# Kernel tuning notes

Measured on AMD Instinct MI355X. Metric: run time of the kernel, lower is better.

## Reference

```python
import jax, jax.numpy as jnp
import numpy as np
from jax import lax

B, T, V, E, H, M = 512, 60, 50000, 300, 512, 256


def _lstm_final_h(x_emb, seqlen, kernel, bias):
    """BasicLSTMCell (gate order i,j,f,o; forget_bias=1.0) with dynamic_rnn
    sequence_length semantics: state stops updating at t >= seqlen.
    x_emb: [B, T, E]; returns final h: [B, H]."""
    b = x_emb.shape[0]
    h0 = jnp.zeros((b, H), x_emb.dtype)
    c0 = jnp.zeros((b, H), x_emb.dtype)

    def step(carry, inp):
        c, h = carry
        xt, t = inp
        z = jnp.concatenate([xt, h], axis=1) @ kernel + bias  # [B, 4H]
        i, j, f, o = jnp.split(z, 4, axis=1)
        nc = c * jax.nn.sigmoid(f + 1.0) + jax.nn.sigmoid(i) * jnp.tanh(j)
        nh = jnp.tanh(nc) * jax.nn.sigmoid(o)
        valid = (t < seqlen)[:, None]
        return (jnp.where(valid, nc, c), jnp.where(valid, nh, h)), None

    (c, h), _ = lax.scan(step, (c0, h0),
                         (jnp.swapaxes(x_emb, 0, 1), jnp.arange(T)))
    return h


def setup_inputs() -> dict:
    key = jax.random.key(0)
    ks = jax.random.split(key, 8)
    return {
        "input1": jax.random.randint(ks[0], (B, T), 0, V, dtype=jnp.int32),
        "input2": jax.random.randint(ks[1], (B, T), 0, V, dtype=jnp.int32),
        "seqlen1": jax.random.randint(ks[2], (B,), 1, T + 1, dtype=jnp.int32),
        "seqlen2": jax.random.randint(ks[3], (B,), 1, T + 1, dtype=jnp.int32),
        "embeddings": jax.random.normal(ks[4], (V, E), jnp.float32) * 0.1,
        "lstm_kernel": jax.random.normal(ks[5], (E + H, 4 * H), jnp.float32) * 0.02,
        "lstm_bias": jnp.zeros((4 * H,), jnp.float32),
        "W1": jax.random.normal(ks[6], (4 * (H + 1) + 1, M), jnp.float32) * 0.02,
        "b1": jnp.zeros((1, M), jnp.float32),
        "W2": jax.random.normal(ks[7], (M, 2), jnp.float32) * 0.02,
        "b2": jnp.zeros((1, 2), jnp.float32),
    }


def reference(input1, input2, seqlen1, seqlen2, embeddings,
              lstm_kernel, lstm_bias, W1, b1, W2, b2):
    x1 = embeddings[input1]  # [B, T, E]
    x2 = embeddings[input2]
    h1 = _lstm_final_h(x1, seqlen1, lstm_kernel, lstm_bias)  # [B, H]
    h2 = _lstm_final_h(x2, seqlen2, lstm_kernel, lstm_bias)
    len1 = (seqlen1.astype(jnp.float32) / float(T))[:, None]
    len2 = (seqlen2.astype(jnp.float32) / float(T))[:, None]
    h1 = jnp.concatenate([h1, len1], axis=1)  # [B, H+1]
    h2 = jnp.concatenate([h2, len2], axis=1)
    h_sub = h1 - h2
    h_dist = jnp.sum(h_sub * h_sub, axis=1, keepdims=True)  # [B, 1]
    h_mul = h1 * h2
    h_combined = jnp.concatenate([h1, h2, h_sub, h_dist, h_mul], axis=1)
    e1 = jax.nn.relu(h_combined @ W1 + b1)  # dropout keep_prob=1 -> identity
    preds = e1 @ W2 + b2  # [B, 2]
    return preds
```

## Files before the change

kernel.cpp:

```cpp
#include <hip/hip_runtime.h>
#include <hip/hip_bf16.h>

#define BATCH 512
#define TT 60
#define EDIM 300
#define HDIM 512
#define KP1 2112
#define MDIM 256
#define V48 2400000

typedef __bf16 bf16x4 __attribute__((ext_vector_type(4)));
typedef __bf16 bf16x8 __attribute__((ext_vector_type(8)));
typedef float  f32x16 __attribute__((ext_vector_type(16)));

#define GLL16(g, l) __builtin_amdgcn_global_load_lds( \
    (const __attribute__((address_space(1))) void*)(g), \
    (__attribute__((address_space(3))) void*)(l), 16, 0, 0)

#define SBAR()  __builtin_amdgcn_s_barrier()
#define SCHED0() __builtin_amdgcn_sched_barrier(0)

__device__ __forceinline__ float sigm(float x) {
    return 1.0f / (1.0f + __expf(-x));
}
__device__ __forceinline__ float tanh_fast(float x) {
    float e = __expf(-2.0f * fabsf(x));
    float r = (1.0f - e) / (1.0f + e);
    return x >= 0.0f ? r : -r;
}


__global__ __launch_bounds__(256) void sort_rows(const int* __restrict__ sl1,
                                                 const int* __restrict__ sl2,
                                                 int* __restrict__ rowinfo,
                                                 unsigned* __restrict__ step_done) {
    __shared__ unsigned cnt[61];
    __shared__ unsigned off[61];
    int tid = threadIdx.x;
    if (tid < 61) cnt[tid] = 0;
    if (tid >= 64 && tid < 80) step_done[tid - 64] = 0;
    __syncthreads();
    for (int i = tid; i < 1024; i += 256) {
        int sl = (i < 512) ? sl1[i] : sl2[i - 512];
        atomicAdd(&cnt[60 - sl], 1u);
    }
    __syncthreads();
    if (tid == 0) {
        unsigned s = 0;
        for (int k = 0; k < 61; ++k) { off[k] = s; s += cnt[k]; }
    }
    __syncthreads();
    for (int i = tid; i < 1024; i += 256) {
        int sc = i >= 512;
        int b = i & 511;
        int sl = sc ? sl2[b] : sl1[b];
        unsigned pos = atomicAdd(&off[60 - sl], 1u);
        rowinfo[pos] = b | (sc << 15) | (sl << 20);
    }
}

__global__ __launch_bounds__(256) void prep_w(const float* __restrict__ kern,
                                              __bf16* __restrict__ wf) {
    __shared__ float tile[64][65];
    int bk = blockIdx.x % 14;
    int bn = blockIdx.x / 14;
    int k0 = bk * 64, n0 = bn * 64;
    int tid = threadIdx.x;
#pragma unroll
    for (int i = 0; i < 16; ++i) {
        int id = i * 256 + tid;
        int kk = id >> 6, nn = id & 63;
        int kg = k0 + kk;
        int src = (kg < 300) ? kg : (kg >= 384 ? kg - 84 : -1);
        tile[kk][nn] = (src >= 0) ? kern[(size_t)src * 2048 + n0 + nn] : 0.0f;
    }
    __syncthreads();
    int gate = n0 >> 9;
    int nt = gate >> 1;
#pragma unroll
    for (int i = 0; i < 2; ++i) {
        int id = i * 256 + tid;
        int nn = id >> 3, k8 = id & 7;
        bf16x8 hv, lv;
#pragma unroll
        for (int j = 0; j < 8; ++j) {
            float v = tile[k8 * 8 + j][nn];
            __bf16 h = (__bf16)v;
            hv[j] = h;
            lv[j] = (__bf16)(v - (float)h);
        }
        int cg = (((n0 & 511) >> 4) + (nn >> 4));
        int hc = nn & 15;
        int lzc = ((gate & 1) << 4) + hc;
        int kglob = k0 + k8 * 8;
        int c = kglob >> 7;
        int j = (kglob >> 4) & 7;
        int half = k8 & 1;
        size_t o = (size_t)cg * 114688 + c * 16384 + (j * 4 + nt * 2) * 512
                 + (half * 32 + lzc) * 8;
        *(bf16x8*)(wf + o) = hv;
        *(bf16x8*)(wf + o + 512) = lv;
    }
}

__global__ __launch_bounds__(256) void prep_w1(const float* __restrict__ W1,
                                               __bf16* __restrict__ w1h,
                                               __bf16* __restrict__ w1l) {
    __shared__ float tile[64][65];
    int bk = blockIdx.x % 33;
    int bn = blockIdx.x / 33;
    int k0 = bk * 64, n0 = bn * 64;
    int tid = threadIdx.x;
#pragma unroll
    for (int i = 0; i < 16; ++i) {
        int id = i * 256 + tid;
        int kk = id >> 6, nn = id & 63;
        int kg = k0 + kk;
        tile[kk][nn] = (kg < 2053) ? W1[(size_t)kg * MDIM + n0 + nn] : 0.0f;
    }
    __syncthreads();
#pragma unroll
    for (int i = 0; i < 2; ++i) {
        int id = i * 256 + tid;
        int nn = id >> 3, k8 = (id & 7) * 8;
        bf16x8 hv, lv;
#pragma unroll
        for (int j = 0; j < 8; ++j) {
            float v = tile[k8 + j][nn];
            __bf16 h = (__bf16)v;
            hv[j] = h;
            lv[j] = (__bf16)(v - (float)h);
        }
        size_t o = (size_t)(n0 + nn) * KP1 + k0 + k8;
        *(bf16x8*)(w1h + o) = hv;
        *(bf16x8*)(w1l + o) = lv;
    }
}

__global__ __launch_bounds__(256) void prep_emb(const float* __restrict__ emb,
                                                __bf16* __restrict__ embB) {
    int id = blockIdx.x * 256 + threadIdx.x;
    if (id >= V48) return;
    int tok = id / 48;
    int k8 = id - tok * 48;
    int k0 = k8 * 8;
    float vv[8];
    const float* er = emb + (size_t)tok * EDIM + k0;
    if (k0 + 8 <= EDIM) {
        float4 f0 = *(const float4*)er;
        float4 f1 = *(const float4*)(er + 4);
        vv[0] = f0.x; vv[1] = f0.y; vv[2] = f0.z; vv[3] = f0.w;
        vv[4] = f1.x; vv[5] = f1.y; vv[6] = f1.z; vv[7] = f1.w;
    } else if (k0 < EDIM) {
        float4 f0 = *(const float4*)er;
        vv[0] = f0.x; vv[1] = f0.y; vv[2] = f0.z; vv[3] = f0.w;
        vv[4] = vv[5] = vv[6] = vv[7] = 0.f;
    } else {
#pragma unroll
        for (int j = 0; j < 8; ++j) vv[j] = 0.f;
    }
    bf16x8 hv, lv;
#pragma unroll
    for (int j = 0; j < 8; ++j) {
        __bf16 h = (__bf16)vv[j];
        hv[j] = h;
        lv[j] = (__bf16)(vv[j] - (float)h);
    }
    size_t o = (size_t)tok * 768 + k0;
    *(bf16x8*)(embB + o) = hv;
    *(bf16x8*)(embB + o + 384) = lv;
}

#define ZSTR 72

__global__ __launch_bounds__(256, 2) void lstm_all(
    const int* __restrict__ in1, const int* __restrict__ in2,
    const int* __restrict__ rowinfo,
    const __bf16* __restrict__ embB, const float* __restrict__ bias,
    const __bf16* __restrict__ wf,
    __bf16* __restrict__ XfH,
    unsigned* __restrict__ step_done,
    float* __restrict__ h_state) {

    int bx = blockIdx.x;
    int xcd = bx & 7;
    int loc = bx >> 3;
    int u = loc >> 3;
    int p = xcd & 1;
    int bt = (u < 4) ? ((u << 1) | p) : (15 - (((u - 4) << 1) | p));
    int cg = ((xcd >> 1) << 3) | (loc & 7);

    __shared__ __align__(16) __bf16 Bb[2][16384];
    __shared__ __align__(16) __bf16 zh[2048];
    __shared__ int info_s[64];

    int tid = threadIdx.x;
    int w = tid >> 6, lane = tid & 63, l31 = lane & 31;
    int s = w >> 1, kg = w & 1;

    if (tid < 64) info_s[tid] = rowinfo[bt * 64 + tid];
    __syncthreads();
    int t_end = info_s[0] >> 20;

    int rowl = s * 32 + l31;
    int inf_r = info_s[rowl];
    const int* tokptr = ((((inf_r >> 15) & 1) ? in2 : in1)) + (inf_r & 511) * TT;

    int hc16 = tid & 15;
    int hcol = (cg << 4) + hc16;
    float bi = bias[hcol], bj = bias[512 + hcol];
    float bfv = bias[1024 + hcol], bo = bias[1536 + hcol];

    float c_reg[4] = {0.f, 0.f, 0.f, 0.f};
    float h_reg[4] = {0.f, 0.f, 0.f, 0.f};

    const __bf16* wb = wf + (size_t)cg * 114688;
    auto stageB = [&](int c, int buf) {
        const __bf16* src = wb + c * 16384 + w * 4096 + lane * 8;
        __bf16* dst = &Bb[buf][w * 4096 + lane * 8];
#pragma unroll
        for (int i = 0; i < 8; ++i)
            GLL16(src + i * 512, dst + i * 512);
    };

    int ew = kg * 64 + ((lane >> 5) << 3);
    size_t hw_off = (size_t)((s * 2 + kg) * 4) * 4096 + lane * 8;

    int tok = tokptr[0];
    stageB(0, 0);
    SCHED0();
    bf16x8 aH[4], aL[4];
    const __bf16* eb = embB + (size_t)tok * 768 + ew;
#pragma unroll
    for (int jj = 0; jj < 4; ++jj) {
        aH[jj] = *(const bf16x8*)(eb + jj * 16);
        aL[jj] = *(const bf16x8*)(eb + 384 + jj * 16);
    }
    SCHED0();

    for (int t = 0; t < t_end; ++t) {
        f32x16 acc[2];
#pragma unroll
        for (int nt = 0; nt < 2; ++nt)
#pragma unroll
            for (int r = 0; r < 16; ++r) acc[nt][r] = 0.0f;

        const __bf16* hrd = XfH + ((size_t)t * 16 + bt) * 65536 + hw_off;

#pragma unroll
        for (int c = 0; c < 7; ++c) {
            int cur = (t + c) & 1;
            asm volatile("s_waitcnt vmcnt(8)" ::: "memory");
            SBAR();
            SCHED0();
            if (c == 2 && t > 0) {
                if (tid == 0) {
                    unsigned target = 32u * (unsigned)t;
                    int guard = 0;
                    while (__hip_atomic_load(step_done + bt, __ATOMIC_RELAXED,
                                             __HIP_MEMORY_SCOPE_AGENT) < target) {
                        __builtin_amdgcn_s_sleep(1);
                        if (++guard > (1 << 20)) break;
                    }
                }
                SBAR();
                SCHED0();
            }
            bf16x8 nH[4], nL[4];
            if (c < 6) {
                stageB(c + 1, 1 - cur);
                SCHED0();
                if (c < 2) {
                    const __bf16* en = eb + (c + 1) * 128;
#pragma unroll
                    for (int jj = 0; jj < 4; ++jj) {
                        nH[jj] = *(const bf16x8*)(en + jj * 16);
                        nL[jj] = *(const bf16x8*)(en + 384 + jj * 16);
                    }
                } else {
                    const __bf16* An = hrd + (c - 2) * 4096;
#pragma unroll
                    for (int jj = 0; jj < 4; ++jj) {
                        nH[jj] = *(const bf16x8*)(An + jj * 1024);
                        nL[jj] = *(const bf16x8*)(An + jj * 1024 + 512);
                    }
                }
                SCHED0();
            }
#pragma unroll
            for (int jj = 0; jj < 4; ++jj) {
                int j = kg * 4 + jj;
#pragma unroll
                for (int nt = 0; nt < 2; ++nt) {
                    int T0 = (j * 4 + nt * 2) * 512 + lane * 8;
                    bf16x8 bh = *(const bf16x8*)(&Bb[cur][T0]);
                    bf16x8 bl = *(const bf16x8*)(&Bb[cur][T0 + 512]);
                    acc[nt] = __builtin_amdgcn_mfma_f32_32x32x16_bf16(aH[jj], bh, acc[nt], 0, 0, 0);
                    acc[nt] = __builtin_amdgcn_mfma_f32_32x32x16_bf16(aH[jj], bl, acc[nt], 0, 0, 0);
                    acc[nt] = __builtin_amdgcn_mfma_f32_32x32x16_bf16(aL[jj], bh, acc[nt], 0, 0, 0);
                }
            }
            if (c < 6) {
#pragma unroll
                for (int jj = 0; jj < 4; ++jj) { aH[jj] = nH[jj]; aL[jj] = nL[jj]; }
            }
        }

        SBAR();
        SCHED0();

        int tn = (t + 1 < TT) ? t + 1 : TT - 1;
        int tok_n = tokptr[tn];
        SCHED0();

        float* zsb = (float*)&Bb[0][0];
#pragma unroll
        for (int nt = 0; nt < 2; ++nt)
#pragma unroll
            for (int r = 0; r < 16; ++r) {
                int rl = s * 32 + (r & 3) + ((r >> 2) << 3) + ((lane >> 5) << 2);
                zsb[kg * 4608 + rl * ZSTR + nt * 32 + l31] = acc[nt][r];
            }
        asm volatile("s_waitcnt lgkmcnt(0)" ::: "memory");
        SBAR();
        SCHED0();

#pragma unroll
        for (int i = 0; i < 4; ++i) {
            int rl = i * 16 + (tid >> 4);
            int info = info_s[rl];
            int sl = info >> 20;
            float zi = zsb[rl * ZSTR + hc16]      + zsb[4608 + rl * ZSTR + hc16]      + bi;
            float zj = zsb[rl * ZSTR + 16 + hc16] + zsb[4608 + rl * ZSTR + 16 + hc16] + bj;
            float zf = zsb[rl * ZSTR + 32 + hc16] + zsb[4608 + rl * ZSTR + 32 + hc16] + bfv;
            float zo = zsb[rl * ZSTR + 48 + hc16] + zsb[4608 + rl * ZSTR + 48 + hc16] + bo;
            float c_old = c_reg[i];
            float h_old = h_reg[i];
            float nc = c_old * sigm(zf + 1.0f) + sigm(zi) * tanh_fast(zj);
            float nh = tanh_fast(nc) * sigm(zo);
            bool valid = t < sl;
            float cs = valid ? nc : c_old;
            float hs = valid ? nh : h_old;
            c_reg[i] = cs;
            h_reg[i] = hs;
            __bf16 hh = (__bf16)hs;
            int grp = hc16 >> 3, e = hc16 & 7;
            zh[(grp * 64 + rl) * 8 + e] = hh;
            zh[((2 + grp) * 64 + rl) * 8 + e] = (__bf16)(hs - (float)hh);
        }
        asm volatile("s_waitcnt lgkmcnt(0)" ::: "memory");
        SBAR();
        SCHED0();

        if (t + 1 < t_end) {
            int plane = tid >> 7;
            int grp = (tid >> 6) & 1;
            int rl = tid & 63;
            ulonglong2 uv = *(const ulonglong2*)(zh + ((plane * 2 + grp) * 64 + rl) * 8);
            int s2 = rl >> 5;
            size_t base = ((size_t)(t + 1) * 16 + bt) * 65536
                        + (size_t)((s2 * 2 + ((cg >> 2) & 1)) * 4 + (cg >> 3)) * 4096
                        + (cg & 3) * 1024 + plane * 512 + (grp * 32 + (rl & 31)) * 8;
            unsigned long long* dst = (unsigned long long*)(XfH + base);
            __hip_atomic_store(dst,     uv.x, __ATOMIC_RELAXED, __HIP_MEMORY_SCOPE_AGENT);
            __hip_atomic_store(dst + 1, uv.y, __ATOMIC_RELAXED, __HIP_MEMORY_SCOPE_AGENT);
            SCHED0();
            stageB(0, (t + 1) & 1);
            SCHED0();
            eb = embB + (size_t)tok_n * 768 + ew;
#pragma unroll
            for (int jj = 0; jj < 4; ++jj) {
                aH[jj] = *(const bf16x8*)(eb + jj * 16);
                aL[jj] = *(const bf16x8*)(eb + 384 + jj * 16);
            }
            SCHED0();
            asm volatile("s_waitcnt vmcnt(16)" ::: "memory");
            SBAR();
            if (tid == 0)
                __hip_atomic_fetch_add(step_done + bt, 1u, __ATOMIC_RELAXED,
                                       __HIP_MEMORY_SCOPE_AGENT);
        }
    }

#pragma unroll
    for (int i = 0; i < 4; ++i) {
        int rl = i * 16 + (tid >> 4);
        int info = info_s[rl];
        int b = info & 511, sc = (info >> 15) & 1;
        h_state[(size_t)((sc << 9) + b) * HDIM + hcol] = h_reg[i];
    }
}

__global__ __launch_bounds__(256) void head1(const float* __restrict__ h_state,
                                             const int* __restrict__ sl1,
                                             const int* __restrict__ sl2,
                                             __bf16* __restrict__ hch,
                                             __bf16* __restrict__ hcl) {
    int b = blockIdx.x;
    int tid = threadIdx.x;
    const float* h1 = h_state + (size_t)b * HDIM;
    const float* h2 = h_state + (size_t)(512 + b) * HDIM;
    size_t ro = (size_t)b * KP1;
    float l1 = (float)sl1[b] / (float)TT;
    float l2 = (float)sl2[b] / (float)TT;
    float part = 0.0f;
#pragma unroll
    for (int i = 0; i < 2; ++i) {
        int k = i * 256 + tid;
        float a = h1[k], c = h2[k];
        float sv = a - c;
        float mv = a * c;
        __bf16 xh;
        xh = (__bf16)a;  hch[ro + k] = xh;         hcl[ro + k] = (__bf16)(a - (float)xh);
        xh = (__bf16)c;  hch[ro + 513 + k] = xh;   hcl[ro + 513 + k] = (__bf16)(c - (float)xh);
        xh = (__bf16)sv; hch[ro + 1026 + k] = xh;  hcl[ro + 1026 + k] = (__bf16)(sv - (float)xh);
        xh = (__bf16)mv; hch[ro + 1540 + k] = xh;  hcl[ro + 1540 + k] = (__bf16)(mv - (float)xh);
        part += sv * sv;
    }
    __shared__ float red[4];
#pragma unroll
    for (int off = 32; off > 0; off >>= 1) part += __shfl_down(part, off, 64);
    if ((tid & 63) == 0) red[tid >> 6] = part;
    __syncthreads();
    if (tid == 0) {
        float d = red[0] + red[1] + red[2] + red[3];
        float ls = l1 - l2;
        d += ls * ls;
        float vals[5] = {l1, l2, ls, d, l1 * l2};
        int pos[5] = {512, 1025, 1538, 1539, 2052};
#pragma unroll
        for (int i = 0; i < 5; ++i) {
            __bf16 xh = (__bf16)vals[i];
            hch[ro + pos[i]] = xh;
            hcl[ro + pos[i]] = (__bf16)(vals[i] - (float)xh);
        }
    }
}

__global__ __launch_bounds__(512, 2) void head2m(
    const __bf16* __restrict__ hch, const __bf16* __restrict__ hcl,
    const __bf16* __restrict__ w1h, const __bf16* __restrict__ w1l,
    float* __restrict__ part) {

    __shared__ __align__(16) __bf16 Bb[2][64 * 512];

    int tid = threadIdx.x;
    int bx = blockIdx.x;
    int mt = bx >> 3;
    int n2 = (bx >> 2) & 1;
    int ks = bx & 3;
    int w = tid >> 6, lane = tid & 63, l31 = lane & 31;
    int half8 = (lane >> 5) << 3;
    int s = w >> 1, nh = w & 1;
    int kbase = ks * 528;

    int k8 = tid & 15;
    int jb = k8 >> 1;
    int rb = (tid >> 4) & 31;
    size_t gboff[8];
    int lo[8];
#pragma unroll
    for (int i = 0; i < 8; ++i) {
        int r = ((i & 3) << 5) + rb;
        int plane = i >> 2;
        int ng = n2 * 128 + r;
        gboff[i] = (size_t)ng * KP1 + k8 * 8;
        int nt = r >> 5;
        int colp = ((r & 31) + (jb << 2)) & 31;
        lo[i] = ((((jb << 2) + nt) << 1) + plane) * 512 + (colp + ((k8 & 1) << 5)) * 8;
    }

    const __bf16* Ah0 = hch + (size_t)(mt * 128 + s * 32 + l31) * KP1 + kbase + half8;
    const __bf16* Al0 = hcl + (size_t)(mt * 128 + s * 32 + l31) * KP1 + kbase + half8;

    bf16x8 rB[8];
    f32x16 acc[2];
#pragma unroll
    for (int nt = 0; nt < 2; ++nt)
#pragma unroll
        for (int r = 0; r < 16; ++r) acc[nt][r] = 0.0f;

#pragma unroll
    for (int i = 0; i < 8; ++i)
        rB[i] = *(const bf16x8*)(((i >= 4) ? w1l : w1h) + gboff[i] + kbase);
#pragma unroll
    for (int i = 0; i < 8; ++i) *(bf16x8*)(&Bb[0][lo[i]]) = rB[i];
    __syncthreads();

    for (int c = 0; c < 5; ++c) {
        int cur = c & 1;
        if (c < 4) {
            int k0 = kbase + (c + 1) * 128;
            bool tail = (c + 1 == 4);
#pragma unroll
            for (int i = 0; i < 8; ++i) {
                if (!tail || k8 < 2)
                    rB[i] = *(const bf16x8*)(((i >= 4) ? w1l : w1h) + gboff[i] + k0);
            }
        }
        int jmax = (c == 4) ? 1 : 8;
        for (int j = 0; j < jmax; ++j) {
            bf16x8 ah = *(const bf16x8*)(Ah0 + c * 128 + j * 16);
            bf16x8 al = *(const bf16x8*)(Al0 + c * 128 + j * 16);
            int cp = ((l31 + (j << 2)) & 31) + ((lane >> 5) << 5);
#pragma unroll
            for (int ntl = 0; ntl < 2; ++ntl) {
                int ntg = nh * 2 + ntl;
                const __bf16* bp = &Bb[cur][(((j << 2) + ntg) << 1) * 512 + cp * 8];
                bf16x8 bh = *(const bf16x8*)bp;
                bf16x8 bl = *(const bf16x8*)(bp + 512);
                acc[ntl] = __builtin_amdgcn_mfma_f32_32x32x16_bf16(ah, bh, acc[ntl], 0, 0, 0);
                acc[ntl] = __builtin_amdgcn_mfma_f32_32x32x16_bf16(ah, bl, acc[ntl], 0, 0, 0);
                acc[ntl] = __builtin_amdgcn_mfma_f32_32x32x16_bf16(al, bh, acc[ntl], 0, 0, 0);
            }
        }
        if (c < 4) {
#pragma unroll
            for (int i = 0; i < 8; ++i) *(bf16x8*)(&Bb[1 - cur][lo[i]]) = rB[i];
        }
        __syncthreads();
    }

#pragma unroll
    for (int ntl = 0; ntl < 2; ++ntl)
#pragma unroll
        for (int r = 0; r < 16; ++r) {
            int row = mt * 128 + s * 32 + (r & 3) + ((r >> 2) << 3) + ((lane >> 5) << 2);
            int col = n2 * 128 + nh * 64 + ntl * 32 + l31;
            part[((size_t)ks * 512 + row) * MDIM + col] = acc[ntl][r];
        }
}

__global__ __launch_bounds__(256) void head3(const float* __restrict__ part,
                                             const float* __restrict__ b1,
                                             const float* __restrict__ W2,
                                             const float* __restrict__ b2,
                                             float* __restrict__ out) {
    int row = blockIdx.x;
    int tid = threadIdx.x;
    float sv = b1[tid];
#pragma unroll
    for (int ks = 0; ks < 4; ++ks)
        sv += part[((size_t)ks * 512 + row) * MDIM + tid];
    float e = fmaxf(sv, 0.0f);
    float p0 = e * W2[tid * 2 + 0];
    float p1 = e * W2[tid * 2 + 1];
#pragma unroll
    for (int off = 32; off > 0; off >>= 1) {
        p0 += __shfl_down(p0, off, 64);
        p1 += __shfl_down(p1, off, 64);
    }
    __shared__ float r0[4], r1[4];
    if ((tid & 63) == 0) { r0[tid >> 6] = p0; r1[tid >> 6] = p1; }
    __syncthreads();
    if (tid == 0) out[row * 2 + 0] = r0[0] + r0[1] + r0[2] + r0[3] + b2[0];
    if (tid == 1) out[row * 2 + 1] = r1[0] + r1[1] + r1[2] + r1[3] + b2[1];
}

extern "C" void kernel_launch(void* const* d_in, const int* in_sizes, int n_in,
                              void* d_out, int out_size, void* d_ws, size_t ws_size,
                              hipStream_t stream) {
    const int*   in1  = (const int*)d_in[0];
    const int*   in2  = (const int*)d_in[1];
    const int*   sl1  = (const int*)d_in[2];
    const int*   sl2  = (const int*)d_in[3];
    const float* emb  = (const float*)d_in[4];
    const float* kern = (const float*)d_in[5];
    const float* bias = (const float*)d_in[6];
    const float* W1   = (const float*)d_in[7];
    const float* b1   = (const float*)d_in[8];
    const float* W2   = (const float*)d_in[9];
    const float* b2   = (const float*)d_in[10];
    float* out = (float*)d_out;

    char* ws = (char*)d_ws;
    int*      rowinfo   = (int*)ws;
    unsigned* step_done = (unsigned*)(ws + 4096u);
    float*  h_state = (float*)(ws + 2097152u);
    __bf16* wf   = (__bf16*)(ws + 6291456u);
    __bf16* hch  = (__bf16*)(ws + 13631488u);
    __bf16* hcl  = (__bf16*)(ws + 15794176u);
    __bf16* w1h  = (__bf16*)(ws + 17956864u);
    __bf16* w1l  = (__bf16*)(ws + 19038208u);
    float*  part = (float*)(ws + 20119552u);
    __bf16* embB = (__bf16*)(ws + 23068672u);
    __bf16* XfH  = (__bf16*)(ws + 100663296u);

    hipMemsetAsync(ws + 13631488u, 0, 4325376u, stream);
    hipMemsetAsync(ws + 100663296u, 0, 2097152u, stream);

    sort_rows<<<dim3(1), dim3(256), 0, stream>>>(sl1, sl2, rowinfo, step_done);
    prep_w<<<dim3(14 * 32), dim3(256), 0, stream>>>(kern, wf);
    prep_w1<<<dim3(33 * 4), dim3(256), 0, stream>>>(W1, w1h, w1l);
    prep_emb<<<dim3(9375), dim3(256), 0, stream>>>(emb, embB);

    lstm_all<<<dim3(512), dim3(256), 0, stream>>>(
        in1, in2, rowinfo, embB, bias, wf, XfH, step_done, h_state);

    head1<<<dim3(512), dim3(256), 0, stream>>>(h_state, sl1, sl2, hch, hcl);
    head2m<<<dim3(32), dim3(512), 0, stream>>>(hch, hcl, w1h, w1l, part);
    head3<<<dim3(512), dim3(256), 0, stream>>>(part, b1, W2, b2, out);
}
```

Before: 1.233 ms.

## Widen LSTM column groups to 32 hidden units with 512-thread persistent blocks

The persistent LSTM kernel now runs 256 blocks of 512 threads instead of 512 blocks of 256. Each block covers 32 hidden columns across all four gates and splits K into 14 chunks of 64, staged through a 4-deep LDS ring with loads issued three chunks ahead. The prepacked weight layout, the hidden-state exchange layout and the step barrier target (16 blocks per batch tile instead of 32) change to match. The aim is to halve cross-block synchronisation traffic and deepen prefetch so more load latency is hidden. The cost is one block per CU with a larger LDS footprint, and a longer sequential K loop per wave.

```diff
diff --git a/kernel.cpp b/kernel.cpp
--- a/kernel.cpp
+++ b/kernel.cpp
@@ -8,6 +8,7 @@
 #define KP1 2112
 #define MDIM 256
 #define V48 2400000
+#define WCG 229376
 
 typedef __bf16 bf16x4 __attribute__((ext_vector_type(4)));
 typedef __bf16 bf16x8 __attribute__((ext_vector_type(8)));
@@ -76,7 +77,6 @@
     }
     __syncthreads();
     int gate = n0 >> 9;
-    int nt = gate >> 1;
 #pragma unroll
     for (int i = 0; i < 2; ++i) {
         int id = i * 256 + tid;
@@ -89,15 +89,14 @@
             hv[j] = h;
             lv[j] = (__bf16)(v - (float)h);
         }
-        int cg = (((n0 & 511) >> 4) + (nn >> 4));
-        int hc = nn & 15;
-        int lzc = ((gate & 1) << 4) + hc;
+        int cg = ((n0 & 511) >> 5) + (nn >> 5);
+        int hc = nn & 31;
         int kglob = k0 + k8 * 8;
-        int c = kglob >> 7;
-        int j = (kglob >> 4) & 7;
-        int half = k8 & 1;
-        size_t o = (size_t)cg * 114688 + c * 16384 + (j * 4 + nt * 2) * 512
-                 + (half * 32 + lzc) * 8;
+        int cc = kglob >> 6;
+        int jp = (kglob >> 4) & 3;
+        int half = (kglob >> 3) & 1;
+        int slot = (jp * 4 + gate) * 2;
+        size_t o = ((size_t)(cg * 14 + cc) * 32 + slot) * 512 + (half * 32 + hc) * 8;
         *(bf16x8*)(wf + o) = hv;
         *(bf16x8*)(wf + o + 512) = lv;
     }
@@ -171,9 +170,9 @@
     *(bf16x8*)(embB + o + 384) = lv;
 }
 
-#define ZSTR 72
-
-__global__ __launch_bounds__(256, 2) void lstm_all(
+#define ZST 136
+
+__global__ __launch_bounds__(512, 1) void lstm_all(
     const int* __restrict__ in1, const int* __restrict__ in2,
     const int* __restrict__ rowinfo,
     const __bf16* __restrict__ embB, const float* __restrict__ bias,
@@ -185,18 +184,17 @@
     int bx = blockIdx.x;
     int xcd = bx & 7;
     int loc = bx >> 3;
-    int u = loc >> 3;
-    int p = xcd & 1;
-    int bt = (u < 4) ? ((u << 1) | p) : (15 - (((u - 4) << 1) | p));
-    int cg = ((xcd >> 1) << 3) | (loc & 7);
-
-    __shared__ __align__(16) __bf16 Bb[2][16384];
-    __shared__ __align__(16) __bf16 zh[2048];
+    int cg = xcd * 2 + (loc >> 4);
+    int bt = loc & 15;
+
+    __shared__ __align__(16) __bf16 Bb[4][16384];
+    __shared__ __align__(16) __bf16 zh[4096];
     __shared__ int info_s[64];
 
     int tid = threadIdx.x;
     int w = tid >> 6, lane = tid & 63, l31 = lane & 31;
-    int s = w >> 1, kg = w & 1;
+    int s = w >> 2, kg = (w >> 1) & 1, n = w & 1;
+    int half8 = (lane >> 5) << 3;
 
     if (tid < 64) info_s[tid] = rowinfo[bt * 64 + tid];
     __syncthreads();
@@ -206,56 +204,74 @@
     int inf_r = info_s[rowl];
     const int* tokptr = ((((inf_r >> 15) & 1) ? in2 : in1)) + (inf_r & 511) * TT;
 
-    int hc16 = tid & 15;
-    int hcol = (cg << 4) + hc16;
+    int hcB = tid & 31;
+    int hcol = cg * 32 + hcB;
     float bi = bias[hcol], bj = bias[512 + hcol];
     float bfv = bias[1024 + hcol], bo = bias[1536 + hcol];
 
     float c_reg[4] = {0.f, 0.f, 0.f, 0.f};
     float h_reg[4] = {0.f, 0.f, 0.f, 0.f};
 
-    const __bf16* wb = wf + (size_t)cg * 114688;
-    auto stageB = [&](int c, int buf) {
-        const __bf16* src = wb + c * 16384 + w * 4096 + lane * 8;
-        __bf16* dst = &Bb[buf][w * 4096 + lane * 8];
-#pragma unroll
-        for (int i = 0; i < 8; ++i)
+    const __bf16* wb = wf + (size_t)cg * WCG;
+    auto stageB = [&](int cc) {
+        const __bf16* src = wb + cc * 16384 + w * 2048 + lane * 8;
+        __bf16* dst = &Bb[cc & 3][w * 2048 + lane * 8];
+#pragma unroll
+        for (int i = 0; i < 4; ++i)
             GLL16(src + i * 512, dst + i * 512);
     };
 
-    int ew = kg * 64 + ((lane >> 5) << 3);
-    size_t hw_off = (size_t)((s * 2 + kg) * 4) * 4096 + lane * 8;
-
-    int tok = tokptr[0];
-    stageB(0, 0);
-    SCHED0();
-    bf16x8 aH[4], aL[4];
-    const __bf16* eb = embB + (size_t)tok * 768 + ew;
-#pragma unroll
-    for (int jj = 0; jj < 4; ++jj) {
-        aH[jj] = *(const bf16x8*)(eb + jj * 16);
-        aL[jj] = *(const bf16x8*)(eb + 384 + jj * 16);
-    }
-    SCHED0();
+    bf16x8 aH[3][2], aL[3][2];
+    const __bf16* eb;
+    const __bf16* hrd;
+
+    auto loadA = [&](int cc, int set) {
+        if (cc < 6) {
+#pragma unroll
+            for (int q = 0; q < 2; ++q) {
+                aH[set][q] = *(const bf16x8*)(eb + cc * 64 + q * 16);
+                aL[set][q] = *(const bf16x8*)(eb + 384 + cc * 64 + q * 16);
+            }
+        } else {
+            int kgL = (cc - 6) & 1, c3 = (cc - 6) >> 1;
+            const __bf16* p = hrd + ((s * 2 + kgL) * 4 + c3) * 4096 + kg * 2048;
+#pragma unroll
+            for (int q = 0; q < 2; ++q) {
+                aH[set][q] = *(const bf16x8*)(p + q * 1024);
+                aL[set][q] = *(const bf16x8*)(p + q * 1024 + 512);
+            }
+        }
+    };
+
+    {
+        int tok = tokptr[0];
+        eb = embB + (size_t)tok * 768 + kg * 32 + half8;
+        hrd = XfH + (size_t)bt * 65536 + lane * 8;
+        stageB(0); stageB(1); stageB(2);
+        SCHED0();
+        loadA(0, 0); loadA(1, 1);
+        SCHED0();
+    }
+
+    float* zs = (float*)&Bb[0][0];
 
     for (int t = 0; t < t_end; ++t) {
         f32x16 acc[2];
 #pragma unroll
-        for (int nt = 0; nt < 2; ++nt)
-#pragma unroll
-            for (int r = 0; r < 16; ++r) acc[nt][r] = 0.0f;
-
-        const __bf16* hrd = XfH + ((size_t)t * 16 + bt) * 65536 + hw_off;
-
-#pragma unroll
-        for (int c = 0; c < 7; ++c) {
-            int cur = (t + c) & 1;
-            asm volatile("s_waitcnt vmcnt(8)" ::: "memory");
+        for (int gg = 0; gg < 2; ++gg)
+#pragma unroll
+            for (int r = 0; r < 16; ++r) acc[gg][r] = 0.0f;
+
+#pragma unroll
+        for (int cc = 0; cc < 14; ++cc) {
+            if (cc == 0)      asm volatile("s_waitcnt vmcnt(16)" ::: "memory");
+            else if (cc == 2) asm volatile("s_waitcnt vmcnt(24)" ::: "memory");
+            else              asm volatile("s_waitcnt vmcnt(20)" ::: "memory");
             SBAR();
             SCHED0();
-            if (c == 2 && t > 0) {
+            if (cc == 4 && t > 0) {
                 if (tid == 0) {
-                    unsigned target = 32u * (unsigned)t;
+                    unsigned target = 16u * (unsigned)t;
                     int guard = 0;
                     while (__hip_atomic_load(step_done + bt, __ATOMIC_RELAXED,
                                              __HIP_MEMORY_SCOPE_AGENT) < target) {
@@ -266,60 +282,34 @@
                 SBAR();
                 SCHED0();
             }
-            bf16x8 nH[4], nL[4];
-            if (c < 6) {
-                stageB(c + 1, 1 - cur);
-                SCHED0();
-                if (c < 2) {
-                    const __bf16* en = eb + (c + 1) * 128;
-#pragma unroll
-                    for (int jj = 0; jj < 4; ++jj) {
-                        nH[jj] = *(const bf16x8*)(en + jj * 16);
-                        nL[jj] = *(const bf16x8*)(en + 384 + jj * 16);
-                    }
-                } else {
-                    const __bf16* An = hrd + (c - 2) * 4096;
-#pragma unroll
-                    for (int jj = 0; jj < 4; ++jj) {
-                        nH[jj] = *(const bf16x8*)(An + jj * 1024);
-                        nL[jj] = *(const bf16x8*)(An + jj * 1024 + 512);
-                    }
+            if (cc <= 10) { stageB(cc + 3); SCHED0(); }
+            if (cc <= 11) { loadA(cc + 2, (cc + 2) % 3); SCHED0(); }
+#pragma unroll
+            for (int q = 0; q < 2; ++q) {
+#pragma unroll
+                for (int gg = 0; gg < 2; ++gg) {
+                    int slot = ((2 * kg + q) * 4 + (2 * n + gg)) * 2;
+                    const __bf16* bp = &Bb[cc & 3][slot * 512 + lane * 8];
+                    bf16x8 bh = *(const bf16x8*)bp;
+                    bf16x8 bl = *(const bf16x8*)(bp + 512);
+                    acc[gg] = __builtin_amdgcn_mfma_f32_32x32x16_bf16(aH[cc % 3][q], bh, acc[gg], 0, 0, 0);
+                    acc[gg] = __builtin_amdgcn_mfma_f32_32x32x16_bf16(aH[cc % 3][q], bl, acc[gg], 0, 0, 0);
+                    acc[gg] = __builtin_amdgcn_mfma_f32_32x32x16_bf16(aL[cc % 3][q], bh, acc[gg], 0, 0, 0);
                 }
-                SCHED0();
-            }
-#pragma unroll
-            for (int jj = 0; jj < 4; ++jj) {
-                int j = kg * 4 + jj;
-#pragma unroll
-                for (int nt = 0; nt < 2; ++nt) {
-                    int T0 = (j * 4 + nt * 2) * 512 + lane * 8;
-                    bf16x8 bh = *(const bf16x8*)(&Bb[cur][T0]);
-                    bf16x8 bl = *(const bf16x8*)(&Bb[cur][T0 + 512]);
-                    acc[nt] = __builtin_amdgcn_mfma_f32_32x32x16_bf16(aH[jj], bh, acc[nt], 0, 0, 0);
-                    acc[nt] = __builtin_amdgcn_mfma_f32_32x32x16_bf16(aH[jj], bl, acc[nt], 0, 0, 0);
-                    acc[nt] = __builtin_amdgcn_mfma_f32_32x32x16_bf16(aL[jj], bh, acc[nt], 0, 0, 0);
-                }
-            }
-            if (c < 6) {
-#pragma unroll
-                for (int jj = 0; jj < 4; ++jj) { aH[jj] = nH[jj]; aL[jj] = nL[jj]; }
             }
         }
 
         SBAR();
         SCHED0();
 
-        int tn = (t + 1 < TT) ? t + 1 : TT - 1;
-        int tok_n = tokptr[tn];
-        SCHED0();
-
-        float* zsb = (float*)&Bb[0][0];
-#pragma unroll
-        for (int nt = 0; nt < 2; ++nt)
+#pragma unroll
+        for (int gg = 0; gg < 2; ++gg)
 #pragma unroll
             for (int r = 0; r < 16; ++r) {
-                int rl = s * 32 + (r & 3) + ((r >> 2) << 3) + ((lane >> 5) << 2);
-                zsb[kg * 4608 + rl * ZSTR + nt * 32 + l31] = acc[nt][r];
+                int row = (r & 3) + ((r >> 2) << 3) + ((lane >> 5) << 2);
+                int zrow = s * 32 + row;
+                int col = (2 * n + gg) * 32 + l31;
+                zs[(kg * 64 + zrow) * ZST + col] = acc[gg][r];
             }
         asm volatile("s_waitcnt lgkmcnt(0)" ::: "memory");
         SBAR();
@@ -327,13 +317,13 @@
 
 #pragma unroll
         for (int i = 0; i < 4; ++i) {
-            int rl = i * 16 + (tid >> 4);
+            int rl = i * 16 + (tid >> 5);
             int info = info_s[rl];
             int sl = info >> 20;
-            float zi = zsb[rl * ZSTR + hc16]      + zsb[4608 + rl * ZSTR + hc16]      + bi;
-            float zj = zsb[rl * ZSTR + 16 + hc16] + zsb[4608 + rl * ZSTR + 16 + hc16] + bj;
-            float zf = zsb[rl * ZSTR + 32 + hc16] + zsb[4608 + rl * ZSTR + 32 + hc16] + bfv;
-            float zo = zsb[rl * ZSTR + 48 + hc16] + zsb[4608 + rl * ZSTR + 48 + hc16] + bo;
+            float zi = zs[rl * ZST + hcB]            + zs[(64 + rl) * ZST + hcB]            + bi;
+            float zj = zs[rl * ZST + 32 + hcB]       + zs[(64 + rl) * ZST + 32 + hcB]       + bj;
+            float zf = zs[rl * ZST + 64 + hcB]       + zs[(64 + rl) * ZST + 64 + hcB]       + bfv;
+            float zo = zs[rl * ZST + 96 + hcB]       + zs[(64 + rl) * ZST + 96 + hcB]       + bo;
             float c_old = c_reg[i];
             float h_old = h_reg[i];
             float nc = c_old * sigm(zf + 1.0f) + sigm(zi) * tanh_fast(zj);
@@ -344,37 +334,39 @@
             c_reg[i] = cs;
             h_reg[i] = hs;
             __bf16 hh = (__bf16)hs;
-            int grp = hc16 >> 3, e = hc16 & 7;
-            zh[(grp * 64 + rl) * 8 + e] = hh;
-            zh[((2 + grp) * 64 + rl) * 8 + e] = (__bf16)(hs - (float)hh);
+            zh[rl * 32 + hcB] = hh;
+            zh[2048 + rl * 32 + hcB] = (__bf16)(hs - (float)hh);
         }
         asm volatile("s_waitcnt lgkmcnt(0)" ::: "memory");
         SBAR();
         SCHED0();
 
         if (t + 1 < t_end) {
-            int plane = tid >> 7;
-            int grp = (tid >> 6) & 1;
-            int rl = tid & 63;
-            ulonglong2 uv = *(const ulonglong2*)(zh + ((plane * 2 + grp) * 64 + rl) * 8);
-            int s2 = rl >> 5;
-            size_t base = ((size_t)(t + 1) * 16 + bt) * 65536
-                        + (size_t)((s2 * 2 + ((cg >> 2) & 1)) * 4 + (cg >> 3)) * 4096
-                        + (cg & 3) * 1024 + plane * 512 + (grp * 32 + (rl & 31)) * 8;
-            unsigned long long* dst = (unsigned long long*)(XfH + base);
-            __hip_atomic_store(dst,     uv.x, __ATOMIC_RELAXED, __HIP_MEMORY_SCOPE_AGENT);
-            __hip_atomic_store(dst + 1, uv.y, __ATOMIC_RELAXED, __HIP_MEMORY_SCOPE_AGENT);
+            int tok_n = tokptr[t + 1];
             SCHED0();
-            stageB(0, (t + 1) & 1);
+            {
+                int rl = tid & 63;
+                int q  = (tid >> 6) & 1;
+                int plane = (tid >> 7) & 1;
+                int hf = (tid >> 8) & 1;
+                ulonglong2 uv = *(const ulonglong2*)(zh + plane * 2048 + rl * 32 + q * 16 + hf * 8);
+                int s2 = rl >> 5, rb = rl & 31;
+                int kgL = (cg >> 1) & 1, c3 = cg >> 2, jj = (cg & 1) * 2 + q;
+                size_t off = ((size_t)(t + 1) * 16 + bt) * 65536
+                           + (size_t)((s2 * 2 + kgL) * 4 + c3) * 4096
+                           + jj * 1024 + plane * 512 + (hf * 32 + rb) * 8;
+                unsigned long long* dst = (unsigned long long*)(XfH + off);
+                __hip_atomic_store(dst,     uv.x, __ATOMIC_RELAXED, __HIP_MEMORY_SCOPE_AGENT);
+                __hip_atomic_store(dst + 1, uv.y, __ATOMIC_RELAXED, __HIP_MEMORY_SCOPE_AGENT);
+            }
             SCHED0();
-            eb = embB + (size_t)tok_n * 768 + ew;
-#pragma unroll
-            for (int jj = 0; jj < 4; ++jj) {
-                aH[jj] = *(const bf16x8*)(eb + jj * 16);
-                aL[jj] = *(const bf16x8*)(eb + 384 + jj * 16);
-            }
+            eb = embB + (size_t)tok_n * 768 + kg * 32 + half8;
+            hrd = XfH + ((size_t)(t + 1) * 16 + bt) * 65536 + lane * 8;
+            stageB(0); stageB(1); stageB(2);
             SCHED0();
-            asm volatile("s_waitcnt vmcnt(16)" ::: "memory");
+            loadA(0, 0); loadA(1, 1);
+            SCHED0();
+            asm volatile("s_waitcnt vmcnt(20)" ::: "memory");
             SBAR();
             if (tid == 0)
                 __hip_atomic_fetch_add(step_done + bt, 1u, __ATOMIC_RELAXED,
@@ -384,7 +376,7 @@
 
 #pragma unroll
     for (int i = 0; i < 4; ++i) {
-        int rl = i * 16 + (tid >> 4);
+        int rl = i * 16 + (tid >> 5);
         int info = info_s[rl];
         int b = info & 511, sc = (info >> 15) & 1;
         h_state[(size_t)((sc << 9) + b) * HDIM + hcol] = h_reg[i];
@@ -594,7 +586,7 @@
     prep_w1<<<dim3(33 * 4), dim3(256), 0, stream>>>(W1, w1h, w1l);
     prep_emb<<<dim3(9375), dim3(256), 0, stream>>>(emb, embB);
 
-    lstm_all<<<dim3(512), dim3(256), 0, stream>>>(
+    lstm_all<<<dim3(256), dim3(512), 0, stream>>>(
         in1, in2, rowinfo, embB, bias, wf, XfH, step_done, h_state);
 
     head1<<<dim3(512), dim3(256), 0, stream>>>(h_state, sl1, sl2, hch, hcl);
```

Measured after the change: 1.442 ms. 17.0% more time.

## Merge two batch tiles per block to share staged LSTM weights

Applied to the files above, without the earlier changes.

Each block of the persistent LSTM kernel now runs 512 threads covering two adjacent batch tiles, so one staged weight chunk in LDS feeds twice as many rows. The grid shrinks to 256 blocks, and step counters and synchronisation are now kept per tile pair. Gate pre-activations move into a dedicated LDS buffer instead of reusing the weight buffer, which lets one barrier go. In exchange, occupancy per CU drops, the pair shares one loop length (the longer tile's), and the old interleaved tile-to-XCD mapping used for load balance is gone.

```diff
diff --git a/kernel.cpp b/kernel.cpp
--- a/kernel.cpp
+++ b/kernel.cpp
@@ -171,9 +171,9 @@
     *(bf16x8*)(embB + o + 384) = lv;
 }
 
-#define ZSTR 72
-
-__global__ __launch_bounds__(256, 2) void lstm_all(
+#define ZSTR 68
+
+__global__ __launch_bounds__(512, 1) void lstm_all(
     const int* __restrict__ in1, const int* __restrict__ in2,
     const int* __restrict__ rowinfo,
     const __bf16* __restrict__ embB, const float* __restrict__ bias,
@@ -185,28 +185,30 @@
     int bx = blockIdx.x;
     int xcd = bx & 7;
     int loc = bx >> 3;
-    int u = loc >> 3;
-    int p = xcd & 1;
-    int bt = (u < 4) ? ((u << 1) | p) : (15 - (((u - 4) << 1) | p));
     int cg = ((xcd >> 1) << 3) | (loc & 7);
+    int pair = ((loc >> 3) << 1) | (xcd & 1);
 
     __shared__ __align__(16) __bf16 Bb[2][16384];
-    __shared__ __align__(16) __bf16 zh[2048];
-    __shared__ int info_s[64];
+    __shared__ float zs[2][2][64][ZSTR];
+    __shared__ __align__(16) __bf16 zh[2][2048];
+    __shared__ int info_s[2][64];
 
     int tid = threadIdx.x;
     int w = tid >> 6, lane = tid & 63, l31 = lane & 31;
-    int s = w >> 1, kg = w & 1;
-
-    if (tid < 64) info_s[tid] = rowinfo[bt * 64 + tid];
-    __syncthreads();
-    int t_end = info_s[0] >> 20;
+    int tg = w >> 2, s = (w >> 1) & 1, kg = w & 1;
+    int bt = pair * 2 + tg;
+
+    if (tid < 128) info_s[tid >> 6][tid & 63] = rowinfo[(pair * 2 + (tid >> 6)) * 64 + (tid & 63)];
+    __syncthreads();
+    int t_end = info_s[0][0] >> 20;
 
     int rowl = s * 32 + l31;
-    int inf_r = info_s[rowl];
+    int inf_r = info_s[tg][rowl];
     const int* tokptr = ((((inf_r >> 15) & 1) ? in2 : in1)) + (inf_r & 511) * TT;
 
-    int hc16 = tid & 15;
+    int tid2 = tid & 255;
+    int tgc = tid >> 8;
+    int hc16 = tid2 & 15;
     int hcol = (cg << 4) + hc16;
     float bi = bias[hcol], bj = bias[512 + hcol];
     float bfv = bias[1024 + hcol], bo = bias[1536 + hcol];
@@ -216,11 +218,11 @@
 
     const __bf16* wb = wf + (size_t)cg * 114688;
     auto stageB = [&](int c, int buf) {
-        const __bf16* src = wb + c * 16384 + w * 4096 + lane * 8;
-        __bf16* dst = &Bb[buf][w * 4096 + lane * 8];
-#pragma unroll
-        for (int i = 0; i < 8; ++i)
-            GLL16(src + i * 512, dst + i * 512);
+        const __bf16* src = wb + c * 16384 + tid * 8;
+        __bf16* dst = &Bb[buf][tid * 8];
+#pragma unroll
+        for (int i = 0; i < 4; ++i)
+            GLL16(src + i * 4096, dst + i * 4096);
     };
 
     int ew = kg * 64 + ((lane >> 5) << 3);
@@ -257,7 +259,7 @@
                 if (tid == 0) {
                     unsigned target = 32u * (unsigned)t;
                     int guard = 0;
-                    while (__hip_atomic_load(step_done + bt, __ATOMIC_RELAXED,
+                    while (__hip_atomic_load(step_done + pair, __ATOMIC_RELAXED,
                                              __HIP_MEMORY_SCOPE_AGENT) < target) {
                         __builtin_amdgcn_s_sleep(1);
                         if (++guard > (1 << 20)) break;
@@ -306,20 +308,16 @@
             }
         }
 
-        SBAR();
-        SCHED0();
-
         int tn = (t + 1 < TT) ? t + 1 : TT - 1;
         int tok_n = tokptr[tn];
         SCHED0();
 
-        float* zsb = (float*)&Bb[0][0];
 #pragma unroll
         for (int nt = 0; nt < 2; ++nt)
 #pragma unroll
             for (int r = 0; r < 16; ++r) {
                 int rl = s * 32 + (r & 3) + ((r >> 2) << 3) + ((lane >> 5) << 2);
-                zsb[kg * 4608 + rl * ZSTR + nt * 32 + l31] = acc[nt][r];
+                zs[tg][kg][rl][nt * 32 + l31] = acc[nt][r];
             }
         asm volatile("s_waitcnt lgkmcnt(0)" ::: "memory");
         SBAR();
@@ -327,13 +325,13 @@
 
 #pragma unroll
         for (int i = 0; i < 4; ++i) {
-            int rl = i * 16 + (tid >> 4);
-            int info = info_s[rl];
+            int rl = i * 16 + (tid2 >> 4);
+            int info = info_s[tgc][rl];
             int sl = info >> 20;
-            float zi = zsb[rl * ZSTR + hc16]      + zsb[4608 + rl * ZSTR + hc16]      + bi;
-            float zj = zsb[rl * ZSTR + 16 + hc16] + zsb[4608 + rl * ZSTR + 16 + hc16] + bj;
-            float zf = zsb[rl * ZSTR + 32 + hc16] + zsb[4608 + rl * ZSTR + 32 + hc16] + bfv;
-            float zo = zsb[rl * ZSTR + 48 + hc16] + zsb[4608 + rl * ZSTR + 48 + hc16] + bo;
+            float zi = zs[tgc][0][rl][hc16]      + zs[tgc][1][rl][hc16]      + bi;
+            float zj = zs[tgc][0][rl][16 + hc16] + zs[tgc][1][rl][16 + hc16] + bj;
+            float zf = zs[tgc][0][rl][32 + hc16] + zs[tgc][1][rl][32 + hc16] + bfv;
+            float zo = zs[tgc][0][rl][48 + hc16] + zs[tgc][1][rl][48 + hc16] + bo;
             float c_old = c_reg[i];
             float h_old = h_reg[i];
             float nc = c_old * sigm(zf + 1.0f) + sigm(zi) * tanh_fast(zj);
@@ -345,25 +343,28 @@
             h_reg[i] = hs;
             __bf16 hh = (__bf16)hs;
             int grp = hc16 >> 3, e = hc16 & 7;
-            zh[(grp * 64 + rl) * 8 + e] = hh;
-            zh[((2 + grp) * 64 + rl) * 8 + e] = (__bf16)(hs - (float)hh);
+            zh[tgc][(grp * 64 + rl) * 8 + e] = hh;
+            zh[tgc][((2 + grp) * 64 + rl) * 8 + e] = (__bf16)(hs - (float)hh);
         }
         asm volatile("s_waitcnt lgkmcnt(0)" ::: "memory");
         SBAR();
         SCHED0();
 
         if (t + 1 < t_end) {
-            int plane = tid >> 7;
-            int grp = (tid >> 6) & 1;
-            int rl = tid & 63;
-            ulonglong2 uv = *(const ulonglong2*)(zh + ((plane * 2 + grp) * 64 + rl) * 8);
-            int s2 = rl >> 5;
-            size_t base = ((size_t)(t + 1) * 16 + bt) * 65536
-                        + (size_t)((s2 * 2 + ((cg >> 2) & 1)) * 4 + (cg >> 3)) * 4096
-                        + (cg & 3) * 1024 + plane * 512 + (grp * 32 + (rl & 31)) * 8;
-            unsigned long long* dst = (unsigned long long*)(XfH + base);
-            __hip_atomic_store(dst,     uv.x, __ATOMIC_RELAXED, __HIP_MEMORY_SCOPE_AGENT);
-            __hip_atomic_store(dst + 1, uv.y, __ATOMIC_RELAXED, __HIP_MEMORY_SCOPE_AGENT);
+            {
+                int plane = (tid2 >> 7) & 1;
+                int grp = (tid2 >> 6) & 1;
+                int rl = tid2 & 63;
+                ulonglong2 uv = *(const ulonglong2*)(&zh[tgc][((plane * 2 + grp) * 64 + rl) * 8]);
+                int s2 = rl >> 5;
+                int bt_p = pair * 2 + tgc;
+                size_t base = ((size_t)(t + 1) * 16 + bt_p) * 65536
+                            + (size_t)((s2 * 2 + ((cg >> 2) & 1)) * 4 + (cg >> 3)) * 4096
+                            + (cg & 3) * 1024 + plane * 512 + (grp * 32 + (rl & 31)) * 8;
+                unsigned long long* dst = (unsigned long long*)(XfH + base);
+                __hip_atomic_store(dst,     uv.x, __ATOMIC_RELAXED, __HIP_MEMORY_SCOPE_AGENT);
+                __hip_atomic_store(dst + 1, uv.y, __ATOMIC_RELAXED, __HIP_MEMORY_SCOPE_AGENT);
+            }
             SCHED0();
             stageB(0, (t + 1) & 1);
             SCHED0();
@@ -374,18 +375,18 @@
                 aL[jj] = *(const bf16x8*)(eb + 384 + jj * 16);
             }
             SCHED0();
-            asm volatile("s_waitcnt vmcnt(16)" ::: "memory");
+            asm volatile("s_waitcnt vmcnt(12)" ::: "memory");
             SBAR();
             if (tid == 0)
-                __hip_atomic_fetch_add(step_done + bt, 1u, __ATOMIC_RELAXED,
+                __hip_atomic_fetch_add(step_done + pair, 1u, __ATOMIC_RELAXED,
                                        __HIP_MEMORY_SCOPE_AGENT);
         }
     }
 
 #pragma unroll
     for (int i = 0; i < 4; ++i) {
-        int rl = i * 16 + (tid >> 4);
-        int info = info_s[rl];
+        int rl = i * 16 + (tid2 >> 4);
+        int info = info_s[tgc][rl];
         int b = info & 511, sc = (info >> 15) & 1;
         h_state[(size_t)((sc << 9) + b) * HDIM + hcol] = h_reg[i];
     }
@@ -594,7 +595,7 @@
     prep_w1<<<dim3(33 * 4), dim3(256), 0, stream>>>(W1, w1h, w1l);
     prep_emb<<<dim3(9375), dim3(256), 0, stream>>>(emb, embB);
 
-    lstm_all<<<dim3(512), dim3(256), 0, stream>>>(
+    lstm_all<<<dim3(256), dim3(512), 0, stream>>>(
         in1, in2, rowinfo, embB, bias, wf, XfH, step_done, h_state);
 
     head1<<<dim3(512), dim3(256), 0, stream>>>(h_state, sl1, sl2, hch, hcl);
```

New measurement: 1.192 ms. 1.03x faster.
